# Optimization experiments

Hardware: AMD Instinct MI355X
Metric: run time of the kernel (lower is better)

The kernel has to match this reference:

```python
import jax, jax.numpy as jnp
import numpy as np


def setup_inputs() -> dict:
    key = jax.random.key(0)
    kA, kB = jax.random.split(key)
    N = 8192
    A = jax.random.normal(kA, (N, N), dtype=jnp.float32)
    B = jax.random.normal(kB, (N, N), dtype=jnp.float32)
    return {"A": A, "B": B}


def reference(A, B):
    # Kernel computes C[i,j] = sum_{k=i..j} A[i,k] * B[k,j] for i <= j, 0 elsewhere.
    # This equals triu(triu(A) @ triu(B)): k>=i is enforced by triu(A),
    # k<=j by triu(B), and output restricted to the upper triangle.
    C = jnp.triu(A) @ jnp.triu(B)
    return jnp.triu(C)
```

## Files before the change

kernel.cpp:

```cpp
#include <hip/hip_runtime.h>
#include <hip/hip_bf16.h>
#include <stdint.h>

static constexpr int ND = 8192;

typedef __attribute__((ext_vector_type(8))) short bf16x8;
typedef __attribute__((ext_vector_type(4))) float f32x4;

#define GLOBAL_AS __attribute__((address_space(1)))
#define LDS_AS __attribute__((address_space(3)))

__device__ __forceinline__ void gld_lds16(const void* g, void* l) {
    __builtin_amdgcn_global_load_lds((const GLOBAL_AS void*)g, (LDS_AS void*)l, 16, 0, 0);
}

__device__ __forceinline__ unsigned short f2bf(float x) {
    union { float f; uint32_t u; } v; v.f = x;
    uint32_t u = v.u;
    uint32_t r = (u + 0x7fffu + ((u >> 16) & 1u)) >> 16;
    return (unsigned short)r;
}

__global__ void conv_a(const float* __restrict__ A, unsigned short* __restrict__ Aw) {
    uint32_t g = blockIdx.x * 256u + threadIdx.x;
    int i  = (int)(g >> 10);
    int k0 = (int)(g & 1023u) << 3;
    if (k0 + 8 <= (i & ~255)) return;
    const float* src = A + (size_t)i * ND + k0;
    f32x4 lo = __builtin_nontemporal_load((const f32x4*)src);
    f32x4 hi = __builtin_nontemporal_load((const f32x4*)(src + 4));
    float vals[8] = {lo[0], lo[1], lo[2], lo[3], hi[0], hi[1], hi[2], hi[3]};
    unsigned short out[8];
#pragma unroll
    for (int e = 0; e < 8; ++e) {
        int k = k0 + e;
        out[e] = (k >= i) ? f2bf(vals[e]) : (unsigned short)0;
    }
    *(uint4*)(Aw + (size_t)i * ND + k0) = *(const uint4*)out;
}

__global__ void conv_bt(const float* __restrict__ B, unsigned short* __restrict__ Bt) {
    __shared__ float tile[64][65];
    int tk = blockIdx.x, tj = blockIdx.y;
    int t = threadIdx.x;
    int k0 = tk * 64, j0 = tj * 64;

    if (k0 > j0 + 63) {
        if (tk >= ((tj >> 2) + 1) * 4) return;
        int jl = t >> 4;
        int kl = (t & 15) * 4;
#pragma unroll
        for (int r = 0; r < 4; ++r) {
            int j = j0 + jl + r * 16;
            *(uint2*)(Bt + (size_t)j * ND + k0 + kl) = make_uint2(0u, 0u);
        }
        return;
    }
    {
        int kl  = t >> 4;
        int jl4 = (t & 15) * 4;
#pragma unroll
        for (int r = 0; r < 4; ++r) {
            int k = k0 + kl + r * 16;
            f32x4 v = __builtin_nontemporal_load(
                (const f32x4*)(B + (size_t)k * ND + j0 + jl4));
            tile[kl + r * 16][jl4 + 0] = v[0];
            tile[kl + r * 16][jl4 + 1] = v[1];
            tile[kl + r * 16][jl4 + 2] = v[2];
            tile[kl + r * 16][jl4 + 3] = v[3];
        }
    }
    __syncthreads();
    {
        int jl  = t >> 4;
        int kl4 = (t & 15) * 4;
#pragma unroll
        for (int r = 0; r < 4; ++r) {
            int j = j0 + jl + r * 16;
            unsigned short o[4];
#pragma unroll
            for (int e = 0; e < 4; ++e) {
                int k = k0 + kl4 + e;
                float v = tile[kl4 + e][jl + r * 16];
                o[e] = (k <= j) ? f2bf(v) : (unsigned short)0;
            }
            *(uint2*)(Bt + (size_t)j * ND + k0 + kl4) = *(const uint2*)o;
        }
    }
}

__global__ __launch_bounds__(256) void zero_lower(float* __restrict__ C) {
    int bid = blockIdx.x;
    int ti = (int)((1.0f + sqrtf(8.0f * (float)bid + 1.0f)) * 0.5f);
    while (ti * (ti + 1) / 2 <= bid) ++ti;
    while (ti * (ti - 1) / 2 > bid) --ti;
    int tj = bid - ti * (ti - 1) / 2;
    if ((ti >> 1) == (tj >> 1)) return;
    int t = threadIdx.x;
    float* base = C + (size_t)(ti * 128) * ND + tj * 128;
    f32x4 z = {0.f, 0.f, 0.f, 0.f};
#pragma unroll
    for (int it = 0; it < 16; ++it) {
        int row = it * 8 + (t >> 5);
        __builtin_nontemporal_store(z, (f32x4*)(base + (size_t)row * ND + (t & 31) * 4));
    }
}

#define BAR() __builtin_amdgcn_s_barrier()
#define WAIT_LGKM0() asm volatile("s_waitcnt lgkmcnt(0)" ::: "memory")
#define WAIT_VM4() asm volatile("s_waitcnt vmcnt(4)" ::: "memory")
#define WAIT_VM0() asm volatile("s_waitcnt vmcnt(0)" ::: "memory")
#define PRIO(x) __builtin_amdgcn_s_setprio(x)

#define LDA(BUF, MH) do { \
    _Pragma("unroll") for (int m_ = 0; m_ < 4; ++m_) \
    _Pragma("unroll") for (int kk_ = 0; kk_ < 2; ++kk_) \
        a_frag[m_][kk_] = *(const bf16x8*)(lds0 + (((BUF)*2 + 0)*2 + (MH))*8192 \
            + (a_lr + m_*16)*64 + (((kk_*4 + khi) ^ lanelo) << 3)); \
} while (0)

#define LDB(BUF, NH) do { \
    _Pragma("unroll") for (int n_ = 0; n_ < 2; ++n_) \
    _Pragma("unroll") for (int kk_ = 0; kk_ < 2; ++kk_) \
        b_frag[NH][n_][kk_] = *(const bf16x8*)(lds0 + (((BUF)*2 + 1)*2 + (NH))*8192 \
            + (b_lr + n_*16)*64 + (((kk_*4 + khi) ^ lanelo) << 3)); \
} while (0)

#define MM(MH, NH) do { \
    _Pragma("unroll") for (int kk_ = 0; kk_ < 2; ++kk_) \
    _Pragma("unroll") for (int m_ = 0; m_ < 4; ++m_) \
    _Pragma("unroll") for (int n_ = 0; n_ < 2; ++n_) \
        acc[(MH)*4 + m_][(NH)*2 + n_] = __builtin_amdgcn_mfma_f32_16x16x32_bf16( \
            a_frag[m_][kk_], b_frag[NH][n_][kk_], acc[(MH)*4 + m_][(NH)*2 + n_], 0, 0, 0); \
} while (0)

__global__ __launch_bounds__(512, 2) void gemm_tri8(const unsigned short* __restrict__ Aw,
                                                    const unsigned short* __restrict__ Bt,
                                                    float* __restrict__ C) {
    int bid = blockIdx.x;
    int s = (int)((sqrtf(8.0f * (float)bid + 1.0f) - 1.0f) * 0.5f);
    while ((s + 1) * (s + 2) / 2 <= bid) ++s;
    while (s * (s + 1) / 2 > bid) --s;
    int tib = bid - s * (s + 1) / 2;
    int tjb = tib + (31 - s);

    __shared__ __align__(16) unsigned short lds[2][2][2][128][64];
    unsigned short* lds0 = &lds[0][0][0][0][0];

    int t = threadIdx.x;
    int lane = t & 63, w = t >> 6;
    int wr = w >> 2, wc = w & 3;
    int lanelo = lane & 7, khi = lane >> 4;
    int a_lr = wr * 64 + (lane & 15);
    int b_lr = wc * 32 + (lane & 15);

    int kstart = tib * 256;
    int nkt = (tjb - tib + 1) * 4;
    int nit = nkt >> 1;

    int srow = w * 8 + (lane >> 3);
    int sg = ((lane & 7) ^ (lane >> 3)) * 8;
    const unsigned short* gA = Aw + (size_t)(tib * 256 + srow) * ND + sg;
    const unsigned short* gB = Bt + (size_t)(tjb * 256 + srow) * ND + sg;
    unsigned short* sdst = lds0 + (w * 512 + lane * 8);

    auto STAGE = [&](int ab, int buf, int h, int ktg) {
        const unsigned short* g = (ab ? gB : gA) + (size_t)(h * 128) * ND + (kstart + ktg * 64);
        unsigned short* l = sdst + ((buf * 2 + ab) * 2 + h) * 8192;
        gld_lds16(g, l);
        gld_lds16(g + (size_t)64 * ND, l + 4096);
    };

    f32x4 acc[8][4];
#pragma unroll
    for (int m = 0; m < 8; ++m)
#pragma unroll
        for (int n = 0; n < 4; ++n) acc[m][n] = (f32x4){0.f, 0.f, 0.f, 0.f};

    bf16x8 a_frag[4][2];
    bf16x8 b_frag[2][2][2];

    STAGE(0, 0, 0, 0); STAGE(1, 0, 0, 0); STAGE(0, 0, 1, 0); STAGE(1, 0, 1, 0);
    STAGE(0, 1, 0, 1); STAGE(1, 1, 0, 1);
    WAIT_VM4();
    BAR();

    for (int I = 0; I < nit; ++I) {
        int k1 = 2 * I + 1, k2 = 2 * I + 2, k3 = 2 * I + 3;
        bool s23 = (k2 < nkt);

        LDA(0, 0); LDB(0, 0);
        STAGE(0, 1, 1, k1);
        BAR(); WAIT_LGKM0(); PRIO(1); MM(0, 0); PRIO(0); BAR();
        LDB(0, 1);
        STAGE(1, 1, 1, k1);
        BAR(); WAIT_LGKM0(); PRIO(1); MM(0, 1); PRIO(0); BAR();
        LDA(0, 1);
        if (s23) STAGE(0, 0, 0, k2);
        BAR(); WAIT_LGKM0(); PRIO(1); MM(1, 0); PRIO(0); BAR();
        if (s23) STAGE(1, 0, 0, k2);
        BAR(); PRIO(1); MM(1, 1); PRIO(0);
        if (s23) { WAIT_VM4(); } else { WAIT_VM0(); }
        BAR();
        LDA(1, 0); LDB(1, 0);
        if (s23) STAGE(0, 0, 1, k2);
        BAR(); WAIT_LGKM0(); PRIO(1); MM(0, 0); PRIO(0); BAR();
        LDB(1, 1);
        if (s23) STAGE(1, 0, 1, k2);
        BAR(); WAIT_LGKM0(); PRIO(1); MM(0, 1); PRIO(0); BAR();
        LDA(1, 1);
        if (s23) STAGE(0, 1, 0, k3);
        BAR(); WAIT_LGKM0(); PRIO(1); MM(1, 0); PRIO(0); BAR();
        if (s23) STAGE(1, 1, 0, k3);
        BAR(); PRIO(1); MM(1, 1); PRIO(0); WAIT_VM4(); BAR();
    }

#pragma unroll
    for (int mh = 0; mh < 2; ++mh)
#pragma unroll
        for (int m = 0; m < 4; ++m)
#pragma unroll
            for (int nh = 0; nh < 2; ++nh)
#pragma unroll
                for (int n = 0; n < 2; ++n) {
                    f32x4 v = acc[mh * 4 + m][nh * 2 + n];
                    int row0 = tib * 256 + mh * 128 + wr * 64 + m * 16 + (lane >> 4) * 4;
                    int col  = tjb * 256 + nh * 128 + wc * 32 + n * 16 + (lane & 15);
#pragma unroll
                    for (int e = 0; e < 4; ++e)
                        __builtin_nontemporal_store(
                            v[e], &C[(size_t)(row0 + e) * ND + col]);
                }
}

__global__ void tri_naive(const float* __restrict__ A, const float* __restrict__ B,
                          float* __restrict__ C) {
    int j = blockIdx.x * 64 + (threadIdx.x & 63);
    int i = blockIdx.y * 4 + (threadIdx.x >> 6);
    float s = 0.f;
    if (j >= i) {
        for (int k = i; k <= j; ++k) s += A[(size_t)i * ND + k] * B[(size_t)k * ND + j];
        C[(size_t)i * ND + j] = s;
    } else {
        C[(size_t)i * ND + j] = 0.f;
    }
}

extern "C" void kernel_launch(void* const* d_in, const int* in_sizes, int n_in,
                              void* d_out, int out_size, void* d_ws, size_t ws_size,
                              hipStream_t stream) {
    (void)in_sizes; (void)n_in; (void)out_size;
    const float* A = (const float*)d_in[0];
    const float* B = (const float*)d_in[1];
    float* C = (float*)d_out;

    const size_t halfws = (size_t)ND * ND * sizeof(unsigned short);
    if (ws_size >= 2 * halfws) {
        unsigned short* Aw = (unsigned short*)d_ws;
        unsigned short* Bt = (unsigned short*)((char*)d_ws + halfws);

        zero_lower<<<dim3(2016), dim3(256), 0, stream>>>(C);
        conv_a<<<dim3(ND * (ND / 8) / 256), dim3(256), 0, stream>>>(A, Aw);
        conv_bt<<<dim3(ND / 64, ND / 64), dim3(256), 0, stream>>>(B, Bt);
        gemm_tri8<<<dim3(528), dim3(512), 0, stream>>>(Aw, Bt, C);
    } else {
        tri_naive<<<dim3(ND / 64, ND / 4), dim3(256), 0, stream>>>(A, B, C);
    }
}
```

Baseline: 333.6 us.

## Replace LDS-staged pipelined GEMM with direct global-to-register fragment loads

Removes the shared-memory double-buffered staging, barriers and priority scheduling from the triangular GEMM and has each wave load its MFMA fragments straight from global memory into registers. The aim is to drop LDS traffic and synchronisation overhead. In exchange, operands that were previously shared across waves through LDS are now re-read from global memory or cache by every wave, and global load latency is no longer hidden by an explicit pipeline.

After: 781.2 us. 134% more time.

```diff
diff --git a/kernel.cpp b/kernel.cpp
--- a/kernel.cpp
+++ b/kernel.cpp
@@ -6,13 +6,6 @@
 
 typedef __attribute__((ext_vector_type(8))) short bf16x8;
 typedef __attribute__((ext_vector_type(4))) float f32x4;
-
-#define GLOBAL_AS __attribute__((address_space(1)))
-#define LDS_AS __attribute__((address_space(3)))
-
-__device__ __forceinline__ void gld_lds16(const void* g, void* l) {
-    __builtin_amdgcn_global_load_lds((const GLOBAL_AS void*)g, (LDS_AS void*)l, 16, 0, 0);
-}
 
 __device__ __forceinline__ unsigned short f2bf(float x) {
     union { float f; uint32_t u; } v; v.f = x;
@@ -106,37 +99,9 @@
     }
 }
 
-#define BAR() __builtin_amdgcn_s_barrier()
-#define WAIT_LGKM0() asm volatile("s_waitcnt lgkmcnt(0)" ::: "memory")
-#define WAIT_VM4() asm volatile("s_waitcnt vmcnt(4)" ::: "memory")
-#define WAIT_VM0() asm volatile("s_waitcnt vmcnt(0)" ::: "memory")
-#define PRIO(x) __builtin_amdgcn_s_setprio(x)
-
-#define LDA(BUF, MH) do { \
-    _Pragma("unroll") for (int m_ = 0; m_ < 4; ++m_) \
-    _Pragma("unroll") for (int kk_ = 0; kk_ < 2; ++kk_) \
-        a_frag[m_][kk_] = *(const bf16x8*)(lds0 + (((BUF)*2 + 0)*2 + (MH))*8192 \
-            + (a_lr + m_*16)*64 + (((kk_*4 + khi) ^ lanelo) << 3)); \
-} while (0)
-
-#define LDB(BUF, NH) do { \
-    _Pragma("unroll") for (int n_ = 0; n_ < 2; ++n_) \
-    _Pragma("unroll") for (int kk_ = 0; kk_ < 2; ++kk_) \
-        b_frag[NH][n_][kk_] = *(const bf16x8*)(lds0 + (((BUF)*2 + 1)*2 + (NH))*8192 \
-            + (b_lr + n_*16)*64 + (((kk_*4 + khi) ^ lanelo) << 3)); \
-} while (0)
-
-#define MM(MH, NH) do { \
-    _Pragma("unroll") for (int kk_ = 0; kk_ < 2; ++kk_) \
-    _Pragma("unroll") for (int m_ = 0; m_ < 4; ++m_) \
-    _Pragma("unroll") for (int n_ = 0; n_ < 2; ++n_) \
-        acc[(MH)*4 + m_][(NH)*2 + n_] = __builtin_amdgcn_mfma_f32_16x16x32_bf16( \
-            a_frag[m_][kk_], b_frag[NH][n_][kk_], acc[(MH)*4 + m_][(NH)*2 + n_], 0, 0, 0); \
-} while (0)
-
-__global__ __launch_bounds__(512, 2) void gemm_tri8(const unsigned short* __restrict__ Aw,
-                                                    const unsigned short* __restrict__ Bt,
-                                                    float* __restrict__ C) {
+__global__ __launch_bounds__(512, 2) void gemm_direct(const unsigned short* __restrict__ Aw,
+                                                      const unsigned short* __restrict__ Bt,
+                                                      float* __restrict__ C) {
     int bid = blockIdx.x;
     int s = (int)((sqrtf(8.0f * (float)bid + 1.0f) - 1.0f) * 0.5f);
     while ((s + 1) * (s + 2) / 2 <= bid) ++s;
@@ -144,75 +109,59 @@
     int tib = bid - s * (s + 1) / 2;
     int tjb = tib + (31 - s);
 
-    __shared__ __align__(16) unsigned short lds[2][2][2][128][64];
-    unsigned short* lds0 = &lds[0][0][0][0][0];
-
     int t = threadIdx.x;
     int lane = t & 63, w = t >> 6;
     int wr = w >> 2, wc = w & 3;
-    int lanelo = lane & 7, khi = lane >> 4;
-    int a_lr = wr * 64 + (lane & 15);
-    int b_lr = wc * 32 + (lane & 15);
+    int khi = lane >> 4;
+    int lr  = lane & 15;
+
+    const unsigned short* arow[8];
+#pragma unroll
+    for (int mh = 0; mh < 2; ++mh)
+#pragma unroll
+        for (int m = 0; m < 4; ++m)
+            arow[mh * 4 + m] =
+                Aw + (size_t)(tib * 256 + mh * 128 + wr * 64 + m * 16 + lr) * ND;
+    const unsigned short* brow[4];
+#pragma unroll
+    for (int nh = 0; nh < 2; ++nh)
+#pragma unroll
+        for (int n = 0; n < 2; ++n)
+            brow[nh * 2 + n] =
+                Bt + (size_t)(tjb * 256 + nh * 128 + wc * 32 + n * 16 + lr) * ND;
+
+    f32x4 acc[8][4];
+#pragma unroll
+    for (int m = 0; m < 8; ++m)
+#pragma unroll
+        for (int n = 0; n < 4; ++n) acc[m][n] = (f32x4){0.f, 0.f, 0.f, 0.f};
 
     int kstart = tib * 256;
     int nkt = (tjb - tib + 1) * 4;
-    int nit = nkt >> 1;
-
-    int srow = w * 8 + (lane >> 3);
-    int sg = ((lane & 7) ^ (lane >> 3)) * 8;
-    const unsigned short* gA = Aw + (size_t)(tib * 256 + srow) * ND + sg;
-    const unsigned short* gB = Bt + (size_t)(tjb * 256 + srow) * ND + sg;
-    unsigned short* sdst = lds0 + (w * 512 + lane * 8);
-
-    auto STAGE = [&](int ab, int buf, int h, int ktg) {
-        const unsigned short* g = (ab ? gB : gA) + (size_t)(h * 128) * ND + (kstart + ktg * 64);
-        unsigned short* l = sdst + ((buf * 2 + ab) * 2 + h) * 8192;
-        gld_lds16(g, l);
-        gld_lds16(g + (size_t)64 * ND, l + 4096);
-    };
-
-    f32x4 acc[8][4];
-#pragma unroll
-    for (int m = 0; m < 8; ++m)
-#pragma unroll
-        for (int n = 0; n < 4; ++n) acc[m][n] = (f32x4){0.f, 0.f, 0.f, 0.f};
-
-    bf16x8 a_frag[4][2];
-    bf16x8 b_frag[2][2][2];
-
-    STAGE(0, 0, 0, 0); STAGE(1, 0, 0, 0); STAGE(0, 0, 1, 0); STAGE(1, 0, 1, 0);
-    STAGE(0, 1, 0, 1); STAGE(1, 1, 0, 1);
-    WAIT_VM4();
-    BAR();
-
-    for (int I = 0; I < nit; ++I) {
-        int k1 = 2 * I + 1, k2 = 2 * I + 2, k3 = 2 * I + 3;
-        bool s23 = (k2 < nkt);
-
-        LDA(0, 0); LDB(0, 0);
-        STAGE(0, 1, 1, k1);
-        BAR(); WAIT_LGKM0(); PRIO(1); MM(0, 0); PRIO(0); BAR();
-        LDB(0, 1);
-        STAGE(1, 1, 1, k1);
-        BAR(); WAIT_LGKM0(); PRIO(1); MM(0, 1); PRIO(0); BAR();
-        LDA(0, 1);
-        if (s23) STAGE(0, 0, 0, k2);
-        BAR(); WAIT_LGKM0(); PRIO(1); MM(1, 0); PRIO(0); BAR();
-        if (s23) STAGE(1, 0, 0, k2);
-        BAR(); PRIO(1); MM(1, 1); PRIO(0);
-        if (s23) { WAIT_VM4(); } else { WAIT_VM0(); }
-        BAR();
-        LDA(1, 0); LDB(1, 0);
-        if (s23) STAGE(0, 0, 1, k2);
-        BAR(); WAIT_LGKM0(); PRIO(1); MM(0, 0); PRIO(0); BAR();
-        LDB(1, 1);
-        if (s23) STAGE(1, 0, 1, k2);
-        BAR(); WAIT_LGKM0(); PRIO(1); MM(0, 1); PRIO(0); BAR();
-        LDA(1, 1);
-        if (s23) STAGE(0, 1, 0, k3);
-        BAR(); WAIT_LGKM0(); PRIO(1); MM(1, 0); PRIO(0); BAR();
-        if (s23) STAGE(1, 1, 0, k3);
-        BAR(); PRIO(1); MM(1, 1); PRIO(0); WAIT_VM4(); BAR();
+
+#pragma unroll 2
+    for (int kt = 0; kt < nkt; ++kt) {
+        int kb = kstart + kt * 64 + khi * 8;
+
+        bf16x8 bfr[4][2];
+#pragma unroll
+        for (int nn = 0; nn < 4; ++nn)
+#pragma unroll
+            for (int kk = 0; kk < 2; ++kk)
+                bfr[nn][kk] = *(const bf16x8*)(brow[nn] + kb + kk * 32);
+
+#pragma unroll
+        for (int mm = 0; mm < 8; ++mm) {
+            bf16x8 a0 = *(const bf16x8*)(arow[mm] + kb);
+            bf16x8 a1 = *(const bf16x8*)(arow[mm] + kb + 32);
+#pragma unroll
+            for (int nn = 0; nn < 4; ++nn) {
+                acc[mm][nn] = __builtin_amdgcn_mfma_f32_16x16x32_bf16(
+                    a0, bfr[nn][0], acc[mm][nn], 0, 0, 0);
+                acc[mm][nn] = __builtin_amdgcn_mfma_f32_16x16x32_bf16(
+                    a1, bfr[nn][1], acc[mm][nn], 0, 0, 0);
+            }
+        }
     }
 
 #pragma unroll
@@ -262,7 +211,7 @@
         zero_lower<<<dim3(2016), dim3(256), 0, stream>>>(C);
         conv_a<<<dim3(ND * (ND / 8) / 256), dim3(256), 0, stream>>>(A, Aw);
         conv_bt<<<dim3(ND / 64, ND / 64), dim3(256), 0, stream>>>(B, Bt);
-        gemm_tri8<<<dim3(528), dim3(512), 0, stream>>>(Aw, Bt, C);
+        gemm_direct<<<dim3(528), dim3(512), 0, stream>>>(Aw, Bt, C);
     } else {
         tri_naive<<<dim3(ND / 64, ND / 4), dim3(256), 0, stream>>>(A, B, C);
     }
```
